# Kernel optimization log

Hardware: AMD Instinct MI355X
Metric: run time of the kernel (lower is better)

## Reference

```python
import jax, jax.numpy as jnp
import numpy as np

N_NODES = 50000


def gcn_conv(x, edge_index, W, b, n_nodes):
    # PyG GCNConv: add self-loops, symmetric normalization, scatter-add, then bias.
    src = jnp.concatenate([edge_index[0], jnp.arange(n_nodes)])
    dst = jnp.concatenate([edge_index[1], jnp.arange(n_nodes)])
    xw = x @ W  # [N, H]
    deg = jax.ops.segment_sum(jnp.ones_like(dst, dtype=xw.dtype), dst, num_segments=n_nodes)
    dinv = jnp.where(deg > 0, jax.lax.rsqrt(jnp.maximum(deg, 1e-12)), 0.0)
    norm = dinv[src] * dinv[dst]  # [E+N]
    msgs = xw[src] * norm[:, None]  # gather + scale
    out = jax.ops.segment_sum(msgs, dst, num_segments=n_nodes)  # scatter-add
    return out + b


def setup_inputs() -> dict:
    key = jax.random.key(0)
    ks = jax.random.split(key, 12)
    d_in, d_h = 128, 128
    inp = {
        "x": jax.random.normal(ks[0], (N_NODES, d_in), dtype=jnp.float32),
        "edge_index": jax.random.randint(ks[1], (2, 800000), 0, N_NODES, dtype=jnp.int64),
        "conv_W": jax.random.normal(ks[2], (d_in, d_h), dtype=jnp.float32) * 0.05,
        "conv_b": jax.random.normal(ks[3], (d_h,), dtype=jnp.float32) * 0.05,
        "W1": jax.random.normal(ks[4], (d_h, 500), dtype=jnp.float32) * 0.05,
        "b1": jax.random.normal(ks[5], (500,), dtype=jnp.float32) * 0.05,
        "W2": jax.random.normal(ks[6], (500, 500), dtype=jnp.float32) * 0.05,
        "b2": jax.random.normal(ks[7], (500,), dtype=jnp.float32) * 0.05,
        "W3": jax.random.normal(ks[8], (500, 500), dtype=jnp.float32) * 0.05,
        "b3": jax.random.normal(ks[9], (500,), dtype=jnp.float32) * 0.05,
        "Wo": jax.random.normal(ks[10], (500, 1), dtype=jnp.float32) * 0.05,
        "bo": jax.random.normal(ks[11], (1,), dtype=jnp.float32) * 0.05,
    }
    return inp


def reference(x, edge_index, conv_W, conv_b, W1, b1, W2, b2, W3, b3, Wo, bo):
    h = jax.nn.relu(gcn_conv(x, edge_index, conv_W, conv_b, N_NODES))
    h = jax.nn.relu(h @ W1 + b1)
    h = jax.nn.relu(h @ W2 + b2)
    h = jax.nn.relu(h @ W3 + b3)
    return h @ Wo + bo
```

## Files before the change

### kernel.cpp

```cpp
#include <hip/hip_runtime.h>
#include <hip/hip_bf16.h>
#include <hip/hip_fp16.h>

#define NN 50000
#define NE 800000

typedef _Float16 f16;
typedef _Float16 f16x2 __attribute__((ext_vector_type(2)));
typedef _Float16 f16x8 __attribute__((ext_vector_type(8)));
typedef float f32x4 __attribute__((ext_vector_type(4)));

__device__ __forceinline__ void gload16(const f16* g, f16* l) {
    __builtin_amdgcn_global_load_lds(
        (__attribute__((address_space(1))) void*)(void*)g,
        (__attribute__((address_space(3))) void*)(void*)l, 16, 0, 0);
}

__device__ __forceinline__ int detect_mode(const void* ei) {
    const long long* p = (const long long*)ei;
    int ok = 1;
#pragma unroll
    for (int i = 0; i < 8; ++i) {
        long long v = p[i];
        if (v < 0 || v >= NN) ok = 0;
    }
    return ok;
}

__device__ __forceinline__ int edge_at(const void* ei, int mode, int idx) {
    if (mode) return (int)((const long long*)ei)[idx];
    return ((const int*)ei)[idx];
}

#define NBLK 49
__global__ __launch_bounds__(1024)
void scan_blocksum(const int* __restrict__ degi, int* __restrict__ bsum) {
    __shared__ int red[1024];
    int i = blockIdx.x * 1024 + threadIdx.x;
    red[threadIdx.x] = (i < NN) ? degi[i] : 0;
    __syncthreads();
    for (int s = 512; s > 0; s >>= 1) {
        if (threadIdx.x < s) red[threadIdx.x] += red[threadIdx.x + s];
        __syncthreads();
    }
    if (threadIdx.x == 0) bsum[blockIdx.x] = red[0];
}

__global__ __launch_bounds__(1024)
void scan_apply(const int* __restrict__ degi, const int* __restrict__ bsum,
                int* __restrict__ off, float* __restrict__ dinv,
                const float* __restrict__ bo, float* __restrict__ out) {
    __shared__ int tmp[1024];
    __shared__ int base;
    int tid = threadIdx.x;
    if (tid == 0) {
        int a = 0;
        for (int b = 0; b < (int)blockIdx.x; ++b) a += bsum[b];
        base = a;
    }
    int i = blockIdx.x * 1024 + tid;
    int v = (i < NN) ? degi[i] : 0;
    tmp[tid] = v;
    __syncthreads();
    for (int s = 1; s < 1024; s <<= 1) {
        int t = (tid >= s) ? tmp[tid - s] : 0;
        __syncthreads();
        tmp[tid] += t;
        __syncthreads();
    }
    if (i < NN) {
        off[i] = base + tmp[tid] - v;
        dinv[i] = rsqrtf((float)v + 1.0f);
        out[i] = bo[0];
    }
}

__global__ void fill_kernel(const void* ei,
                            const int* __restrict__ off, int* __restrict__ cursor,
                            int* __restrict__ csr) {
    int e = blockIdx.x * blockDim.x + threadIdx.x;
    if (e >= NE) return;
    int mode = detect_mode(ei);
    int s = edge_at(ei, mode, e);
    int d = edge_at(ei, mode, NE + e);
    int pos = atomicAdd(&cursor[d], 1);
    csr[off[d] + pos] = s;
}

__global__ __launch_bounds__(256)
void gather_kernel(const int* __restrict__ csr, const int* __restrict__ off,
                   const int* __restrict__ degi, const f16* __restrict__ xwh,
                   const float* __restrict__ dinv, const float* __restrict__ conv_b,
                   f16* __restrict__ h0h) {
    int wv = threadIdx.x >> 6, lane = threadIdx.x & 63;
    int n = blockIdx.x * 4 + wv;
    if (n >= NN) return;
    int o = off[n], dg = degi[n];
    float ax = 0.f, ay = 0.f, bx = 0.f, by = 0.f;
    int j = 0;
    for (; j + 1 < dg; j += 2) {
        int s0 = csr[o + j], s1 = csr[o + j + 1];
        float d0 = dinv[s0], d1 = dinv[s1];
        f16x2 v0 = *(const f16x2*)(xwh + (size_t)s0 * 128 + lane * 2);
        f16x2 v1 = *(const f16x2*)(xwh + (size_t)s1 * 128 + lane * 2);
        ax += (float)v0[0] * d0; ay += (float)v0[1] * d0;
        bx += (float)v1[0] * d1; by += (float)v1[1] * d1;
    }
    if (j < dg) {
        int s0 = csr[o + j];
        float d0 = dinv[s0];
        f16x2 v0 = *(const f16x2*)(xwh + (size_t)s0 * 128 + lane * 2);
        ax += (float)v0[0] * d0; ay += (float)v0[1] * d0;
    }
    float dn = dinv[n];
    f16x2 vs = *(const f16x2*)(xwh + (size_t)n * 128 + lane * 2);
    float rx = (ax + bx + (float)vs[0] * dn) * dn + conv_b[lane * 2];
    float ry = (ay + by + (float)vs[1] * dn) * dn + conv_b[lane * 2 + 1];
    f16x2 r;
    r[0] = (f16)fmaxf(rx, 0.f);
    r[1] = (f16)fmaxf(ry, 0.f);
    *(f16x2*)(h0h + (size_t)n * 128 + lane * 2) = r;
}

__global__ void prep_all(const float* __restrict__ x, f16* __restrict__ xh,
                         const float* __restrict__ cW, const float* __restrict__ W1,
                         const float* __restrict__ W2, const float* __restrict__ W3,
                         const float* __restrict__ Wo, const float* __restrict__ b1,
                         const float* __restrict__ b2, const float* __restrict__ b3,
                         f16* __restrict__ cWT, f16* __restrict__ W1T,
                         f16* __restrict__ W2T, f16* __restrict__ W3T,
                         float* __restrict__ Wof, float* __restrict__ b1p,
                         float* __restrict__ b2p, float* __restrict__ b3p,
                         const void* ei, int* __restrict__ degi) {
    int i = blockIdx.x * 256 + threadIdx.x;
    if (i < 800000) {
        int e = i * 8;
        float4 u0 = *(const float4*)(x + e);
        float4 u1 = *(const float4*)(x + e + 4);
        f16x8 o;
        o[0] = (f16)u0.x; o[1] = (f16)u0.y; o[2] = (f16)u0.z; o[3] = (f16)u0.w;
        o[4] = (f16)u1.x; o[5] = (f16)u1.y; o[6] = (f16)u1.z; o[7] = (f16)u1.w;
        *(f16x8*)(xh + e) = o;
        return;
    }
    i -= 800000;
    if (i < 16384) { int n = i >> 7, k = i & 127; cWT[i] = (f16)cW[k * 128 + n]; return; }
    i -= 16384;
    if (i < 65536) { int n = i >> 7, k = i & 127; W1T[i] = (f16)((n < 500) ? W1[k * 500 + n] : 0.f); return; }
    i -= 65536;
    if (i < 262144) { int n = i >> 9, k = i & 511; W2T[i] = (f16)((n < 500 && k < 500) ? W2[k * 500 + n] : 0.f); return; }
    i -= 262144;
    if (i < 262144) { int n = i >> 9, k = i & 511; W3T[i] = (f16)((n < 500 && k < 500) ? W3[k * 500 + n] : 0.f); return; }
    i -= 262144;
    if (i < 512) { Wof[i] = (i < 500) ? Wo[i] : 0.f; return; }
    i -= 512;
    if (i < 512) { b1p[i] = (i < 500) ? b1[i] : 0.f; return; }
    i -= 512;
    if (i < 512) { b2p[i] = (i < 500) ? b2[i] : 0.f; return; }
    i -= 512;
    if (i < 512) { b3p[i] = (i < 500) ? b3[i] : 0.f; return; }
    i -= 512;
    if (i < NE) {
        int mode = detect_mode(ei);
        int d = edge_at(ei, mode, NE + i);
        atomicAdd(&degi[d], 1);
    }
}

template <bool SWZ, bool RELU, bool BIAS, bool FUSE>
__global__ __launch_bounds__(256)
void mfma_gemm(const f16* __restrict__ A, const f16* __restrict__ Bt,
               const float* __restrict__ biasp, f16* __restrict__ C,
               const float* __restrict__ Wof, float* __restrict__ out,
               int M, int Npad, int K) {
    int bx, by;
    if (SWZ) {
        int id = blockIdx.x + 4 * blockIdx.y;
        int x = id & 7, s = id >> 3;
        bx = s & 3;
        by = (s >> 2) * 8 + x;
        if (by * 128 >= M) return;
    } else {
        bx = blockIdx.x; by = blockIdx.y;
    }
    __shared__ f16 As[3][4096];
    __shared__ f16 Bs[3][4096];
    const int tid = threadIdx.x;
    const int lane = tid & 63;
    const int wm = (tid >> 6) >> 1, wn = (tid >> 6) & 1;
    const int l15 = lane & 15, lk = lane >> 4;
    const int row0 = by * 128, col0 = bx * 128;

    size_t abase[2], bbase[2];
#pragma unroll
    for (int i = 0; i < 2; ++i) {
        int s = tid + i * 256;
        int m = s >> 2;
        int kgp = (s & 3) ^ (m & 3);
        int row = row0 + m; if (row > M - 1) row = M - 1;
        abase[i] = (size_t)row * K + kgp * 8;
        bbase[i] = (size_t)(col0 + m) * K + kgp * 8;
    }
    const int fragoff = l15 * 32 + ((lk ^ (l15 & 3)) * 8);
    f32x4 acc[4][4] = {};

    const int nt = K >> 5;

#define STAGE(buf, t)                                              \
    {                                                              \
        int _k0 = (t) << 5;                                        \
        _Pragma("unroll")                                          \
        for (int i = 0; i < 2; ++i) {                              \
            gload16(A + abase[i] + _k0, &As[buf][tid * 8 + i * 2048]);  \
            gload16(Bt + bbase[i] + _k0, &Bs[buf][tid * 8 + i * 2048]); \
        }                                                          \
    }

#define COMPUTE(buf)                                               \
    {                                                              \
        f16x8 af[4], bf[4];                                        \
        _Pragma("unroll")                                          \
        for (int f = 0; f < 4; ++f) {                              \
            af[f] = *(const f16x8*)&As[buf][(wm * 64 + f * 16) * 32 + fragoff]; \
            bf[f] = *(const f16x8*)&Bs[buf][(wn * 64 + f * 16) * 32 + fragoff]; \
        }                                                          \
        _Pragma("unroll")                                          \
        for (int fi = 0; fi < 4; ++fi)                             \
            _Pragma("unroll")                                      \
            for (int fj = 0; fj < 4; ++fj)                         \
                acc[fi][fj] = __builtin_amdgcn_mfma_f32_16x16x32_f16( \
                    af[fi], bf[fj], acc[fi][fj], 0, 0, 0);         \
    }

    STAGE(0, 0);
    STAGE(1, 1);

    int cur = 0;
    for (int t = 0; t < nt - 2; ++t) {
        int pb = cur + 2; if (pb >= 3) pb -= 3;
        __builtin_amdgcn_sched_barrier(0);
        __builtin_amdgcn_s_barrier();
        __builtin_amdgcn_sched_barrier(0);
        STAGE(pb, t + 2);
        asm volatile("s_waitcnt vmcnt(8)" ::: "memory");
        __builtin_amdgcn_sched_barrier(0);
        __builtin_amdgcn_s_barrier();
        __builtin_amdgcn_sched_barrier(0);
        COMPUTE(cur);
        cur += 1; if (cur >= 3) cur -= 3;
    }
    {
        __builtin_amdgcn_sched_barrier(0);
        __builtin_amdgcn_s_barrier();
        asm volatile("s_waitcnt vmcnt(4)" ::: "memory");
        __builtin_amdgcn_sched_barrier(0);
        __builtin_amdgcn_s_barrier();
        __builtin_amdgcn_sched_barrier(0);
        COMPUTE(cur);
        cur += 1; if (cur >= 3) cur -= 3;
    }
    {
        __builtin_amdgcn_sched_barrier(0);
        __builtin_amdgcn_s_barrier();
        asm volatile("s_waitcnt vmcnt(0)" ::: "memory");
        __builtin_amdgcn_sched_barrier(0);
        __builtin_amdgcn_s_barrier();
        __builtin_amdgcn_sched_barrier(0);
        COMPUTE(cur);
    }
#undef STAGE
#undef COMPUTE

    if (FUSE) {
#pragma unroll
        for (int fi = 0; fi < 4; ++fi)
#pragma unroll
            for (int r = 0; r < 4; ++r) {
                float part = 0.f;
#pragma unroll
                for (int fj = 0; fj < 4; ++fj) {
                    int n = col0 + wn * 64 + fj * 16 + l15;
                    float v = acc[fi][fj][r];
                    if (BIAS) v += biasp[n];
                    if (RELU) v = fmaxf(v, 0.f);
                    part += v * Wof[n];
                }
                part += __shfl_xor(part, 1, 64);
                part += __shfl_xor(part, 2, 64);
                part += __shfl_xor(part, 4, 64);
                part += __shfl_xor(part, 8, 64);
                int row = row0 + wm * 64 + fi * 16 + lk * 4 + r;
                if (l15 == 0 && row < M) atomicAdd(out + row, part);
            }
    } else {
#pragma unroll
        for (int fi = 0; fi < 4; ++fi)
#pragma unroll
            for (int r = 0; r < 4; ++r) {
                int row = row0 + wm * 64 + fi * 16 + lk * 4 + r;
                if (row < M) {
#pragma unroll
                    for (int fj = 0; fj < 4; ++fj) {
                        int n = col0 + wn * 64 + fj * 16 + l15;
                        float v = acc[fi][fj][r];
                        if (BIAS) v += biasp[n];
                        if (RELU) v = fmaxf(v, 0.f);
                        C[(size_t)row * Npad + n] = (f16)v;
                    }
                }
            }
    }
}

extern "C" void kernel_launch(void* const* d_in, const int* in_sizes, int n_in,
                              void* d_out, int out_size, void* d_ws, size_t ws_size,
                              hipStream_t stream) {
    const float* x      = (const float*)d_in[0];
    const void*  ei     = d_in[1];
    const float* conv_W = (const float*)d_in[2];
    const float* conv_b = (const float*)d_in[3];
    const float* W1 = (const float*)d_in[4];
    const float* b1 = (const float*)d_in[5];
    const float* W2 = (const float*)d_in[6];
    const float* b2 = (const float*)d_in[7];
    const float* W3 = (const float*)d_in[8];
    const float* b3 = (const float*)d_in[9];
    const float* Wo = (const float*)d_in[10];
    const float* bo = (const float*)d_in[11];
    float* out = (float*)d_out;

    char* ws = (char*)d_ws;
    size_t off_b = 0;
    auto alloc = [&](size_t bytes) {
        void* p = ws + off_b;
        off_b = (off_b + bytes + 255) & ~(size_t)255;
        return p;
    };
    f16*   xh   = (f16*)alloc((size_t)NN * 128 * 2);
    f16*   xwh  = (f16*)alloc((size_t)NN * 128 * 2);
    f16*   h0h  = (f16*)alloc((size_t)NN * 128 * 2);
    f16*   h1h  = (f16*)alloc((size_t)NN * 512 * 2);
    f16*   h2h  = (f16*)alloc((size_t)NN * 512 * 2);
    f16*   cWT  = (f16*)alloc(128 * 128 * 2);
    f16*   W1T  = (f16*)alloc(512 * 128 * 2);
    f16*   W2T  = (f16*)alloc(512 * 512 * 2);
    f16*   W3T  = (f16*)alloc(512 * 512 * 2);
    float* Wof  = (float*)alloc(512 * 4);
    float* b1p  = (float*)alloc(512 * 4);
    float* b2p  = (float*)alloc(512 * 4);
    float* b3p  = (float*)alloc(512 * 4);
    int*   degi   = (int*)alloc(NN * 4);
    int*   offn   = (int*)alloc(NN * 4);
    int*   cursor = (int*)alloc(NN * 4);
    float* dinv   = (float*)alloc(NN * 4);
    int*   bsum   = (int*)alloc(NBLK * 4);
    int*   csr    = (int*)alloc((size_t)NE * 4);

    hipMemsetAsync(degi, 0, (size_t)NN * 4, stream);
    hipMemsetAsync(cursor, 0, (size_t)NN * 4, stream);

    prep_all<<<(2208256 + 255) / 256, 256, 0, stream>>>(
        x, xh, conv_W, W1, W2, W3, Wo, b1, b2, b3,
        cWT, W1T, W2T, W3T, Wof, b1p, b2p, b3p, ei, degi);

    mfma_gemm<false, false, false, false><<<dim3(1, 391), 256, 0, stream>>>(
        xh, cWT, nullptr, xwh, nullptr, nullptr, NN, 128, 128);

    scan_blocksum<<<NBLK, 1024, 0, stream>>>(degi, bsum);
    scan_apply<<<NBLK, 1024, 0, stream>>>(degi, bsum, offn, dinv, bo, out);
    fill_kernel<<<(NE + 255) / 256, 256, 0, stream>>>(ei, offn, cursor, csr);
    gather_kernel<<<(NN + 3) / 4, 256, 0, stream>>>(csr, offn, degi, xwh, dinv, conv_b, h0h);

    mfma_gemm<true, true, true, false><<<dim3(4, 392), 256, 0, stream>>>(
        h0h, W1T, b1p, h1h, nullptr, nullptr, NN, 512, 128);
    mfma_gemm<true, true, true, false><<<dim3(4, 392), 256, 0, stream>>>(
        h1h, W2T, b2p, h2h, nullptr, nullptr, NN, 512, 512);
    mfma_gemm<true, true, true, true><<<dim3(4, 392), 256, 0, stream>>>(
        h2h, W3T, b3p, nullptr, Wof, out, NN, 512, 512);
}
```

Before: 353.9 us.

## Template GEMM tiles and use 128x256 tiles with 512 threads for MLP layers

Makes the MFMA GEMM kernel templated on thread count, tile sizes and warp layout. The three MLP GEMMs now use 128x256 output tiles with 8 waves, which cuts redundant A-tile loads per output column. The LDS swizzle gains an extra XOR term to reduce bank conflicts, and the swizzled block mapping and vmcnt wait counts are adjusted to the new load count per thread. Larger tiles mean more LDS per block and fewer blocks, which may lower occupancy. The early-exit bounds check in the swizzle is dropped, and the epilogue code (not shown) must handle the new tile shape.

```diff
diff --git a/kernel.cpp b/kernel.cpp
--- a/kernel.cpp
+++ b/kernel.cpp
@@ -167,53 +167,66 @@
     }
 }
 
-template <bool SWZ, bool RELU, bool BIAS, bool FUSE>
-__global__ __launch_bounds__(256)
+template <int NT, int BM, int BN, int LOG2WN, bool SWZ, bool RELU, bool BIAS, bool FUSE>
+__global__ __launch_bounds__(NT)
 void mfma_gemm(const f16* __restrict__ A, const f16* __restrict__ Bt,
                const float* __restrict__ biasp, f16* __restrict__ C,
                const float* __restrict__ Wof, float* __restrict__ out,
                int M, int Npad, int K) {
+    constexpr int WN = 1 << LOG2WN;
+    constexpr int ASLOTS = BM * 4;
+    constexpr int BSLOTS = BN * 4;
+    constexpr int LPTA = ASLOTS / NT;
+    constexpr int LPTB = BSLOTS / NT;
+    constexpr int LPT = LPTA + LPTB;
+
     int bx, by;
     if (SWZ) {
-        int id = blockIdx.x + 4 * blockIdx.y;
-        int x = id & 7, s = id >> 3;
-        bx = s & 3;
-        by = (s >> 2) * 8 + x;
-        if (by * 128 >= M) return;
+        int id = blockIdx.x + 2 * blockIdx.y;
+        bx = (id >> 3) & 1;
+        by = (id >> 4) * 8 + (id & 7);
     } else {
         bx = blockIdx.x; by = blockIdx.y;
     }
-    __shared__ f16 As[3][4096];
-    __shared__ f16 Bs[3][4096];
+    __shared__ f16 As[3][BM * 32];
+    __shared__ f16 Bs[3][BN * 32];
     const int tid = threadIdx.x;
     const int lane = tid & 63;
-    const int wm = (tid >> 6) >> 1, wn = (tid >> 6) & 1;
+    const int wid = tid >> 6;
+    const int wm = wid >> LOG2WN, wn = wid & (WN - 1);
     const int l15 = lane & 15, lk = lane >> 4;
-    const int row0 = by * 128, col0 = bx * 128;
-
-    size_t abase[2], bbase[2];
-#pragma unroll
-    for (int i = 0; i < 2; ++i) {
-        int s = tid + i * 256;
+    const int row0 = by * BM, col0 = bx * BN;
+
+    size_t abase[LPTA], bbase[LPTB];
+#pragma unroll
+    for (int i = 0; i < LPTA; ++i) {
+        int s = tid + i * NT;
         int m = s >> 2;
-        int kgp = (s & 3) ^ (m & 3);
+        int kgp = (s & 3) ^ (m & 3) ^ ((m >> 2) & 3);
         int row = row0 + m; if (row > M - 1) row = M - 1;
         abase[i] = (size_t)row * K + kgp * 8;
+    }
+#pragma unroll
+    for (int i = 0; i < LPTB; ++i) {
+        int s = tid + i * NT;
+        int m = s >> 2;
+        int kgp = (s & 3) ^ (m & 3) ^ ((m >> 2) & 3);
         bbase[i] = (size_t)(col0 + m) * K + kgp * 8;
     }
-    const int fragoff = l15 * 32 + ((lk ^ (l15 & 3)) * 8);
+    const int fragoff = l15 * 32 + ((lk ^ (l15 & 3) ^ ((l15 >> 2) & 3)) * 8);
     f32x4 acc[4][4] = {};
 
     const int nt = K >> 5;
 
-#define STAGE(buf, t)                                              \
-    {                                                              \
-        int _k0 = (t) << 5;                                        \
-        _Pragma("unroll")                                          \
-        for (int i = 0; i < 2; ++i) {                              \
-            gload16(A + abase[i] + _k0, &As[buf][tid * 8 + i * 2048]);  \
-            gload16(Bt + bbase[i] + _k0, &Bs[buf][tid * 8 + i * 2048]); \
-        }                                                          \
+#define STAGE(buf, t)                                                   \
+    {                                                                   \
+        int _k0 = (t) << 5;                                             \
+        _Pragma("unroll")                                               \
+        for (int i = 0; i < LPTA; ++i)                                  \
+            gload16(A + abase[i] + _k0, &As[buf][(tid + i * NT) * 8]);  \
+        _Pragma("unroll")                                               \
+        for (int i = 0; i < LPTB; ++i)                                  \
+            gload16(Bt + bbase[i] + _k0, &Bs[buf][(tid + i * NT) * 8]); \
     }
 
 #define COMPUTE(buf)                                               \
@@ -242,7 +255,11 @@
         __builtin_amdgcn_s_barrier();
         __builtin_amdgcn_sched_barrier(0);
         STAGE(pb, t + 2);
-        asm volatile("s_waitcnt vmcnt(8)" ::: "memory");
+        if constexpr (LPT == 4) {
+            asm volatile("s_waitcnt vmcnt(8)" ::: "memory");
+        } else {
+            asm volatile("s_waitcnt vmcnt(6)" ::: "memory");
+        }
         __builtin_amdgcn_sched_barrier(0);
         __builtin_amdgcn_s_barrier();
         __builtin_amdgcn_sched_barrier(0);
@@ -252,7 +269,11 @@
     {
         __builtin_amdgcn_sched_barrier(0);
         __builtin_amdgcn_s_barrier();
-        asm volatile("s_waitcnt vmcnt(4)" ::: "memory");
+        if constexpr (LPT == 4) {
+            asm volatile("s_waitcnt vmcnt(4)" ::: "memory");
+        } else {
+            asm volatile("s_waitcnt vmcnt(3)" ::: "memory");
+        }
         __builtin_amdgcn_sched_barrier(0);
         __builtin_amdgcn_s_barrier();
         __builtin_amdgcn_sched_barrier(0);
@@ -363,7 +384,8 @@
         x, xh, conv_W, W1, W2, W3, Wo, b1, b2, b3,
         cWT, W1T, W2T, W3T, Wof, b1p, b2p, b3p, ei, degi);
 
-    mfma_gemm<false, false, false, false><<<dim3(1, 391), 256, 0, stream>>>(
+    mfma_gemm<256, 128, 128, 1, false, false, false, false>
+        <<<dim3(1, 391), 256, 0, stream>>>(
         xh, cWT, nullptr, xwh, nullptr, nullptr, NN, 128, 128);
 
     scan_blocksum<<<NBLK, 1024, 0, stream>>>(degi, bsum);
@@ -371,10 +393,13 @@
     fill_kernel<<<(NE + 255) / 256, 256, 0, stream>>>(ei, offn, cursor, csr);
     gather_kernel<<<(NN + 3) / 4, 256, 0, stream>>>(csr, offn, degi, xwh, dinv, conv_b, h0h);
 
-    mfma_gemm<true, true, true, false><<<dim3(4, 392), 256, 0, stream>>>(
+    mfma_gemm<512, 128, 256, 2, true, true, true, false>
+        <<<dim3(2, 392), 512, 0, stream>>>(
         h0h, W1T, b1p, h1h, nullptr, nullptr, NN, 512, 128);
-    mfma_gemm<true, true, true, false><<<dim3(4, 392), 256, 0, stream>>>(
+    mfma_gemm<512, 128, 256, 2, true, true, true, false>
+        <<<dim3(2, 392), 512, 0, stream>>>(
         h1h, W2T, b2p, h2h, nullptr, nullptr, NN, 512, 512);
-    mfma_gemm<true, true, true, true><<<dim3(4, 392), 256, 0, stream>>>(
+    mfma_gemm<512, 128, 256, 2, true, true, true, true>
+        <<<dim3(2, 392), 512, 0, stream>>>(
         h2h, W3T, b3p, nullptr, Wof, out, NN, 512, 512);
 }
```

Measured after the change: 355.6 us. Within noise of the previous version (+0.5%).
